# Kernel optimization log

Measured on AMD Instinct MI355X. Metric: run time of the kernel, lower is better.

Reference implementation:

```python
import jax, jax.numpy as jnp
import numpy as np

N = 50000   # total nodes across batched graphs
E = 800000  # total edges
F = 30      # input node features
G = 256     # number of graphs in the disjoint batch
CH = [128, 64, 32]
N_LABELS = 2


def setup_inputs() -> dict:
    key = jax.random.key(0)
    ks = jax.random.split(key, 16)
    x = jax.random.normal(ks[0], (N, F), dtype=jnp.float32)
    edge_weight = jax.random.uniform(ks[1], (E,), dtype=jnp.float32)
    edge_row = jax.random.randint(ks[2], (E,), 0, N, dtype=jnp.int32)
    edge_col = jax.random.randint(ks[3], (E,), 0, N, dtype=jnp.int32)
    seg = jnp.sort(jax.random.randint(ks[4], (N,), 0, G, dtype=jnp.int32))
    # GCSConv params: out = A @ (x W1) + x W2 + b, per layer
    dims = [F] + CH
    params = {}
    kk = 5
    for l in range(3):
        fin, fout = dims[l], dims[l + 1]
        s = 1.0 / np.sqrt(fin)
        params[f"w1_{l+1}"] = jax.random.uniform(ks[kk], (fin, fout), minval=-s, maxval=s, dtype=jnp.float32); kk += 1
        params[f"w2_{l+1}"] = jax.random.uniform(ks[kk], (fin, fout), minval=-s, maxval=s, dtype=jnp.float32); kk += 1
        params[f"b_{l+1}"] = jnp.zeros((fout,), dtype=jnp.float32)
    sd = 1.0 / np.sqrt(CH[-1])
    params["wd"] = jax.random.uniform(ks[kk], (CH[-1], N_LABELS), minval=-sd, maxval=sd, dtype=jnp.float32)
    params["bd"] = jnp.zeros((N_LABELS,), dtype=jnp.float32)
    return {"x": x, "edge_weight": edge_weight, "edge_row": edge_row,
            "edge_col": edge_col, "seg": seg, **params}


def _gcs_conv(x, ew, er, ec, w1, w2, b):
    # spektral GCSConv: relu(A @ (x W1) + x W2 + b) with sparse A in COO form
    h = x @ w1                                   # [N, Fout]
    msgs = ew[:, None] * h[ec]                   # gather along edges [E, Fout]
    agg = jax.ops.segment_sum(msgs, er, num_segments=N)  # SpMM scatter [N, Fout]
    return jax.nn.relu(agg + x @ w2 + b)


def reference(x, edge_weight, edge_row, edge_col, seg,
              w1_1, w2_1, b_1, w1_2, w2_2, b_2, w1_3, w2_3, b_3, wd, bd):
    h = _gcs_conv(x, edge_weight, edge_row, edge_col, w1_1, w2_1, b_1)
    h = _gcs_conv(h, edge_weight, edge_row, edge_col, w1_2, w2_2, b_2)
    h = _gcs_conv(h, edge_weight, edge_row, edge_col, w1_3, w2_3, b_3)
    # GlobalAvgPool: segment mean over graph ids
    sums = jax.ops.segment_sum(h, seg, num_segments=G)               # [G, 32]
    cnts = jax.ops.segment_sum(jnp.ones((N,), h.dtype), seg, num_segments=G)
    pooled = sums / jnp.maximum(cnts, 1.0)[:, None]
    return jax.nn.softmax(pooled @ wd + bd, axis=-1)                 # [G, 2]
```

## Files before the change

kernel.cpp:

```cpp
#include <hip/hip_runtime.h>
#include <hip/hip_fp16.h>

#define N_NODES 50000
#define N_EDGES 800000
#define N_GRAPHS 256
#define NCB 196
#define CHUNK 3125
#define MBLK 782

typedef _Float16 f16x8 __attribute__((ext_vector_type(8)));
typedef float    f32x4 __attribute__((ext_vector_type(4)));

__global__ __launch_bounds__(256)
void hist_prep(const int* __restrict__ ER, const float* __restrict__ X,
               const int* __restrict__ SEG,
               const float* __restrict__ W1, const float* __restrict__ W2,
               const float* __restrict__ W12, const float* __restrict__ W22,
               const float* __restrict__ W13, const float* __restrict__ W23,
               int* __restrict__ ghist, __half* __restrict__ XPh,
               int* __restrict__ start,
               __half* __restrict__ W1f, __half* __restrict__ W2f,
               __half* __restrict__ W3f)
{
    int b = blockIdx.x;
    int t = threadIdx.x;
    if (b < 256) {
        __shared__ int h[NCB];
        for (int i = t; i < NCB; i += 256) h[i] = 0;
        __syncthreads();
        int lo = b * CHUNK, hi = lo + CHUNK;
        for (int e = lo + t; e < hi; e += 256) atomicAdd(&h[ER[e] >> 8], 1);
        __syncthreads();
        for (int i = t; i < NCB; i += 256) ghist[i * 256 + b] = h[i];
        return;
    }
    int bid = b - 256;
    if (bid < 6250) {
        int idx = bid * 256 + t;
        int n = idx >> 5;
        int c = idx & 31;
        float v = (c < 30) ? X[n * 30 + c] : 0.f;
        XPh[(size_t)n * 32 + c] = __float2half(v);
    } else if (bid < 6446) {
        int n = (bid - 6250) * 256 + t;
        if (n >= N_NODES) return;
        int g = SEG[n];
        int gprev = (n == 0) ? -1 : SEG[n - 1];
        for (int gg = gprev + 1; gg <= g; ++gg) start[gg] = n;
        if (n == N_NODES - 1)
            for (int gg = g + 1; gg <= N_GRAPHS; ++gg) start[gg] = N_NODES;
    } else {
        int idx = (bid - 6446) * 256 + t;
        if (idx < 8192) {
            int i = idx & 7, c = (idx >> 3) & 15, g = (idx >> 7) & 3;
            int s = (idx >> 9) & 1, n = idx >> 10;
            int k = s * 32 + g * 8 + i, col = n * 16 + c;
            float w = 0.f;
            if (k < 30) w = W1[k * 128 + col];
            else if (k >= 32 && k < 62) w = W2[(k - 32) * 128 + col];
            W1f[idx] = __float2half(w);
        } else if (idx < 24576) {
            int o = idx - 8192;
            int i = o & 7, c = (o >> 3) & 15, g = (o >> 7) & 3;
            int s = (o >> 9) & 3, n = o >> 11;
            int k = s * 32 + g * 8 + i, col = n * 16 + c;
            float w = (col < 64) ? W12[k * 64 + col] : W22[k * 64 + col - 64];
            W2f[o] = __float2half(w);
        } else {
            int o = idx - 24576;
            int i = o & 7, c = (o >> 3) & 15, g = (o >> 7) & 3;
            int s = (o >> 9) & 1, n = o >> 10;
            int k = s * 32 + g * 8 + i, col = n * 16 + c;
            float w = (col < 32) ? W13[k * 32 + col] : W23[k * 32 + col - 32];
            W3f[o] = __float2half(w);
        }
    }
}

__global__ __launch_bounds__(256)
void scan1(int* __restrict__ ghist, int* __restrict__ bsum)
{
    __shared__ int s[256];
    int t = threadIdx.x, b = blockIdx.x;
    int i = b * 256 + t;
    int v = ghist[i];
    s[t] = v;
    __syncthreads();
    for (int off = 1; off < 256; off <<= 1) {
        int u = (t >= off) ? s[t - off] : 0;
        __syncthreads();
        s[t] += u;
        __syncthreads();
    }
    ghist[i] = s[t] - v;
    if (t == 255) bsum[b] = s[255];
}

__global__ __launch_bounds__(256)
void c_scatter(const int* __restrict__ ER, const int* __restrict__ EC,
               const float* __restrict__ EW, const int* __restrict__ ghist,
               const int* __restrict__ bsum, unsigned int* __restrict__ tmp_sd,
               __half* __restrict__ tmp_w)
{
    __shared__ int s[256];
    __shared__ int cur[NCB];
    int t = threadIdx.x, blk = blockIdx.x;
    int v = (t < NCB) ? bsum[t] : 0;
    s[t] = v;
    __syncthreads();
    for (int off = 1; off < 256; off <<= 1) {
        int u = (t >= off) ? s[t - off] : 0;
        __syncthreads();
        s[t] += u;
        __syncthreads();
    }
    if (t < NCB) cur[t] = (s[t] - v) + ghist[t * 256 + blk];
    __syncthreads();
    int lo = blk * CHUNK, hi = lo + CHUNK;
    for (int e = lo + t; e < hi; e += 256) {
        int d = ER[e];
        int pos = atomicAdd(&cur[d >> 8], 1);
        tmp_sd[pos] = (unsigned int)EC[e] | ((unsigned int)(d & 255) << 16);
        tmp_w[pos] = __float2half(EW[e]);
    }
}

__device__ __forceinline__ void fma8h(float4& a0, float4& a1, float w,
                                      const uint4& raw)
{
    const __half2* hp = (const __half2*)&raw;
    float2 f0 = __half22float2(hp[0]);
    float2 f1 = __half22float2(hp[1]);
    float2 f2 = __half22float2(hp[2]);
    float2 f3 = __half22float2(hp[3]);
    a0.x = fmaf(w, f0.x, a0.x); a0.y = fmaf(w, f0.y, a0.y);
    a0.z = fmaf(w, f1.x, a0.z); a0.w = fmaf(w, f1.y, a0.w);
    a1.x = fmaf(w, f2.x, a1.x); a1.y = fmaf(w, f2.y, a1.y);
    a1.z = fmaf(w, f3.x, a1.z); a1.w = fmaf(w, f3.y, a1.w);
}

__device__ __forceinline__ unsigned int relu2(unsigned int u)
{
    unsigned int lo = (u & 0x8000u)     ? 0u : (u & 0x0000FFFFu);
    unsigned int hi = (u & 0x80000000u) ? 0u : (u & 0xFFFF0000u);
    return lo | hi;
}

__global__ __launch_bounds__(1024)
void bsort(const unsigned int* __restrict__ tmp_sd, const __half* __restrict__ tmp_w,
           const int* __restrict__ bsum,
           unsigned int* __restrict__ packed, int* __restrict__ rowptr)
{
    __shared__ int s[256];
    __shared__ int hist[256];
    __shared__ int cur[256];
    int t = threadIdx.x, b = blockIdx.x;

    if (t < 256) s[t] = (t < NCB) ? bsum[t] : 0;
    __syncthreads();
    for (int off = 1; off < 256; off <<= 1) {
        int u = 0;
        if (t < 256 && t >= off) u = s[t - off];
        __syncthreads();
        if (t < 256) s[t] += u;
        __syncthreads();
    }
    int cntb = bsum[b];
    int base = s[b] - cntb;
    int end  = base + cntb;
    __syncthreads();

    if (t < 256) hist[t] = 0;
    __syncthreads();
    for (int j = base + t; j < end; j += 1024)
        atomicAdd(&hist[(tmp_sd[j] >> 16) & 255], 1);
    __syncthreads();
    int hv = 0;
    if (t < 256) { hv = hist[t]; s[t] = hv; }
    __syncthreads();
    for (int off = 1; off < 256; off <<= 1) {
        int u = 0;
        if (t < 256 && t >= off) u = s[t - off];
        __syncthreads();
        if (t < 256) s[t] += u;
        __syncthreads();
    }
    if (t < 256) {
        int excl = s[t] - hv;
        int n = b * 256 + t;
        if (n < N_NODES) rowptr[n] = base + excl;
        if (b == NCB - 1 && t == 0) rowptr[N_NODES] = N_EDGES;
        cur[t] = base + excl;
    }
    __syncthreads();
    for (int j = base + t; j < end; j += 1024) {
        unsigned int sd = tmp_sd[j];
        unsigned short hb = __half_as_ushort(tmp_w[j]);
        int pos = atomicAdd(&cur[(sd >> 16) & 255], 1);
        packed[pos] = (sd & 0xFFFF) | ((unsigned int)hb << 16);
    }
}

__global__ __launch_bounds__(256)
void dense12_mfma(const __half* __restrict__ XPh, const int* __restrict__ rowptr,
                  const unsigned int* __restrict__ packed,
                  const __half* __restrict__ W1f, const float* __restrict__ B1,
                  const __half* __restrict__ W2f, const float* __restrict__ B2,
                  __half* __restrict__ H2h, __half* __restrict__ A2h)
{
    __shared__ __align__(16) __half As[64 * 72];
    __shared__ __align__(16) __half Hs[64 * 136];
    const int tid = threadIdx.x;
    const int m0 = blockIdx.x * 64;
    const int lane = tid & 63;
    const int w  = tid >> 6;
    const int lr = lane & 15;
    const int lg = lane >> 4;

    {
        int row = tid >> 2, c4 = tid & 3;
        int gm = m0 + row;
        uint4 v = make_uint4(0, 0, 0, 0);
        if (gm < N_NODES) v = *(const uint4*)(XPh + (size_t)gm * 32 + c4 * 8);
        *(uint4*)(As + row * 72 + (4 + c4) * 8) = v;
    }
    {
        int local = tid >> 2, q = tid & 3;
        int n = m0 + local;
        __half2 hb2[4];
        if (n < N_NODES) {
            int r0 = rowptr[n], r1 = rowptr[n + 1];
            float4 acc0 = make_float4(0.f, 0.f, 0.f, 0.f);
            float4 acc1 = make_float4(0.f, 0.f, 0.f, 0.f);
            int j = r0;
            for (; j + 3 < r1; j += 4) {
                unsigned int ra = packed[j],     rb = packed[j + 1];
                unsigned int rc = packed[j + 2], rd = packed[j + 3];
                uint4 rawa = *(const uint4*)(XPh + (size_t)(ra & 0xFFFF) * 32 + q * 8);
                uint4 rawb = *(const uint4*)(XPh + (size_t)(rb & 0xFFFF) * 32 + q * 8);
                uint4 rawc = *(const uint4*)(XPh + (size_t)(rc & 0xFFFF) * 32 + q * 8);
                uint4 rawd = *(const uint4*)(XPh + (size_t)(rd & 0xFFFF) * 32 + q * 8);
                float wa = __half2float(__ushort_as_half((unsigned short)(ra >> 16)));
                float wb = __half2float(__ushort_as_half((unsigned short)(rb >> 16)));
                float wc = __half2float(__ushort_as_half((unsigned short)(rc >> 16)));
                float wd = __half2float(__ushort_as_half((unsigned short)(rd >> 16)));
                fma8h(acc0, acc1, wa, rawa);
                fma8h(acc0, acc1, wb, rawb);
                fma8h(acc0, acc1, wc, rawc);
                fma8h(acc0, acc1, wd, rawd);
            }
            for (; j < r1; ++j) {
                unsigned int r = packed[j];
                uint4 raw = *(const uint4*)(XPh + (size_t)(r & 0xFFFF) * 32 + q * 8);
                float wv = __half2float(__ushort_as_half((unsigned short)(r >> 16)));
                fma8h(acc0, acc1, wv, raw);
            }
            hb2[0] = __float22half2_rn(make_float2(acc0.x, acc0.y));
            hb2[1] = __float22half2_rn(make_float2(acc0.z, acc0.w));
            hb2[2] = __float22half2_rn(make_float2(acc1.x, acc1.y));
            hb2[3] = __float22half2_rn(make_float2(acc1.z, acc1.w));
        } else {
            hb2[0] = hb2[1] = hb2[2] = hb2[3] = __float22half2_rn(make_float2(0.f, 0.f));
        }
        *(uint4*)(As + local * 72 + q * 8) = *(uint4*)&hb2[0];
    }
    __syncthreads();

    f32x4 acc[4][2];
    #pragma unroll
    for (int m = 0; m < 4; ++m)
        #pragma unroll
        for (int j = 0; j < 2; ++j)
            acc[m][j] = (f32x4){0.f, 0.f, 0.f, 0.f};

    #pragma unroll
    for (int s = 0; s < 2; ++s) {
        f16x8 a[4];
        #pragma unroll
        for (int m = 0; m < 4; ++m)
            a[m] = *(const f16x8*)(As + (m * 16 + lr) * 72 + s * 32 + lg * 8);
        #pragma unroll
        for (int j = 0; j < 2; ++j) {
            const int n = 2 * w + j;
            f16x8 b = *(const f16x8*)(W1f + (((n * 2 + s) * 4 + lg) * 16 + lr) * 8);
            #pragma unroll
            for (int m = 0; m < 4; ++m)
                acc[m][j] = __builtin_amdgcn_mfma_f32_16x16x32_f16(a[m], b, acc[m][j], 0, 0, 0);
        }
    }

    #pragma unroll
    for (int j = 0; j < 2; ++j) {
        const int n = 2 * w + j;
        const float bias = B1[n * 16 + lr];
        #pragma unroll
        for (int m = 0; m < 4; ++m)
            #pragma unroll
            for (int r = 0; r < 4; ++r) {
                float v = fmaxf(acc[m][j][r] + bias, 0.f);
                Hs[(m * 16 + lg * 4 + r) * 136 + n * 16 + lr] = __float2half(v);
            }
    }
    __syncthreads();

    f32x4 acc2[4][2];
    #pragma unroll
    for (int m = 0; m < 4; ++m)
        #pragma unroll
        for (int j = 0; j < 2; ++j)
            acc2[m][j] = (f32x4){0.f, 0.f, 0.f, 0.f};

    #pragma unroll
    for (int s = 0; s < 4; ++s) {
        f16x8 a[4];
        #pragma unroll
        for (int m = 0; m < 4; ++m)
            a[m] = *(const f16x8*)(Hs + (m * 16 + lr) * 136 + s * 32 + lg * 8);
        #pragma unroll
        for (int j = 0; j < 2; ++j) {
            const int n = 2 * w + j;
            f16x8 b = *(const f16x8*)(W2f + (((n * 4 + s) * 4 + lg) * 16 + lr) * 8);
            #pragma unroll
            for (int m = 0; m < 4; ++m)
                acc2[m][j] = __builtin_amdgcn_mfma_f32_16x16x32_f16(a[m], b, acc2[m][j], 0, 0, 0);
        }
    }
    __syncthreads();

    #pragma unroll
    for (int j = 0; j < 2; ++j) {
        const int n = 2 * w + j;
        const float bias = (n >= 4) ? B2[(n - 4) * 16 + lr] : 0.f;
        #pragma unroll
        for (int m = 0; m < 4; ++m)
            #pragma unroll
            for (int r = 0; r < 4; ++r)
                Hs[(m * 16 + lg * 4 + r) * 136 + n * 16 + lr] =
                    __float2half(acc2[m][j][r] + bias);
    }
    __syncthreads();

    for (int idx = tid; idx < 1024; idx += 256) {
        int row = idx >> 4, c8 = idx & 15;
        int gm = m0 + row;
        if (gm < N_NODES) {
            uint4 v = *(const uint4*)(Hs + row * 136 + c8 * 8);
            if (c8 < 8) *(uint4*)(H2h + (size_t)gm * 64 + c8 * 8) = v;
            else        *(uint4*)(A2h + (size_t)gm * 64 + (c8 - 8) * 8) = v;
        }
    }
}

__global__ __launch_bounds__(256)
void dense3_mfma(const __half* __restrict__ X, const __half* __restrict__ W3f,
                 const float* __restrict__ B3, __half* __restrict__ H3h,
                 __half* __restrict__ B2h)
{
    __shared__ __align__(16) __half As[64 * 72];
    __shared__ __align__(16) __half Os[64 * 72];
    const int tid = threadIdx.x;
    const int m0 = blockIdx.x * 64;
    const int lane = tid & 63;
    const int w  = tid >> 6;
    const int lr = lane & 15;
    const int lg = lane >> 4;

    for (int idx = tid; idx < 512; idx += 256) {
        int row = idx >> 3, c8 = idx & 7;
        int gm = m0 + row;
        uint4 v = make_uint4(0, 0, 0, 0);
        if (gm < N_NODES) v = *(const uint4*)(X + (size_t)gm * 64 + c8 * 8);
        v.x = relu2(v.x); v.y = relu2(v.y); v.z = relu2(v.z); v.w = relu2(v.w);
        *(uint4*)(As + row * 72 + c8 * 8) = v;
    }
    __syncthreads();

    f32x4 acc[4];
    #pragma unroll
    for (int m = 0; m < 4; ++m) acc[m] = (f32x4){0.f, 0.f, 0.f, 0.f};

    #pragma unroll
    for (int s = 0; s < 2; ++s) {
        f16x8 b = *(const f16x8*)(W3f + (((w * 2 + s) * 4 + lg) * 16 + lr) * 8);
        #pragma unroll
        for (int m = 0; m < 4; ++m) {
            f16x8 a = *(const f16x8*)(As + (m * 16 + lr) * 72 + s * 32 + lg * 8);
            acc[m] = __builtin_amdgcn_mfma_f32_16x16x32_f16(a, b, acc[m], 0, 0, 0);
        }
    }

    const float bias = (w >= 2) ? B3[(w - 2) * 16 + lr] : 0.f;
    #pragma unroll
    for (int m = 0; m < 4; ++m)
        #pragma unroll
        for (int r = 0; r < 4; ++r)
            Os[(m * 16 + lg * 4 + r) * 72 + w * 16 + lr] =
                __float2half(acc[m][r] + bias);
    __syncthreads();

    for (int idx = tid; idx < 512; idx += 256) {
        int row = idx >> 3, c8 = idx & 7;
        int gm = m0 + row;
        if (gm < N_NODES) {
            uint4 v = *(const uint4*)(Os + row * 72 + c8 * 8);
            if (c8 < 4) *(uint4*)(H3h + (size_t)gm * 32 + c8 * 8) = v;
            else        *(uint4*)(B2h + (size_t)gm * 32 + (c8 - 4) * 8) = v;
        }
    }
}

template<int FOUT, int S>
__global__ __launch_bounds__(512)
void spmm_split(const __half* __restrict__ H, const int* __restrict__ rowptr,
                const unsigned int* __restrict__ packed, __half* __restrict__ AGGh)
{
    constexpr int T = FOUT / 8;
    constexpr int NPB = 512 / (S * T);
    __shared__ float part[NPB][S - 1][FOUT + 4];
    int tid = threadIdx.x;
    int local = tid / (S * T);
    int rem = tid % (S * T);
    int s = rem / T;
    int q = rem % T;
    int n = blockIdx.x * NPB + local;
    bool valid = (n < N_NODES);
    float4 acc0 = make_float4(0.f, 0.f, 0.f, 0.f);
    float4 acc1 = make_float4(0.f, 0.f, 0.f, 0.f);
    __half* ap = AGGh + (size_t)n * FOUT + q * 8;
    if (valid) {
        int r0 = rowptr[n], r1 = rowptr[n + 1];
        int deg = r1 - r0;
        int lo = r0 + (deg * s) / S;
        int hi = r0 + (deg * (s + 1)) / S;
        if (s == 0) {
            uint4 raw = *(const uint4*)ap;
            const __half2* hp = (const __half2*)&raw;
            float2 f0 = __half22float2(hp[0]);
            float2 f1 = __half22float2(hp[1]);
            float2 f2 = __half22float2(hp[2]);
            float2 f3 = __half22float2(hp[3]);
            acc0 = make_float4(f0.x, f0.y, f1.x, f1.y);
            acc1 = make_float4(f2.x, f2.y, f3.x, f3.y);
        }
        int j = lo;
        for (; j + 3 < hi; j += 4) {
            unsigned int ra = packed[j],     rb = packed[j + 1];
            unsigned int rc = packed[j + 2], rd = packed[j + 3];
            uint4 rawa = *(const uint4*)(H + (size_t)(ra & 0xFFFF) * FOUT + q * 8);
            uint4 rawb = *(const uint4*)(H + (size_t)(rb & 0xFFFF) * FOUT + q * 8);
            uint4 rawc = *(const uint4*)(H + (size_t)(rc & 0xFFFF) * FOUT + q * 8);
            uint4 rawd = *(const uint4*)(H + (size_t)(rd & 0xFFFF) * FOUT + q * 8);
            float wa = __half2float(__ushort_as_half((unsigned short)(ra >> 16)));
            float wb = __half2float(__ushort_as_half((unsigned short)(rb >> 16)));
            float wc = __half2float(__ushort_as_half((unsigned short)(rc >> 16)));
            float wd = __half2float(__ushort_as_half((unsigned short)(rd >> 16)));
            fma8h(acc0, acc1, wa, rawa);
            fma8h(acc0, acc1, wb, rawb);
            fma8h(acc0, acc1, wc, rawc);
            fma8h(acc0, acc1, wd, rawd);
        }
        for (; j < hi; ++j) {
            unsigned int r = packed[j];
            uint4 raw = *(const uint4*)(H + (size_t)(r & 0xFFFF) * FOUT + q * 8);
            float w = __half2float(__ushort_as_half((unsigned short)(r >> 16)));
            fma8h(acc0, acc1, w, raw);
        }
    }
    if (s > 0) {
        *(float4*)&part[local][s - 1][q * 8 + 0] = acc0;
        *(float4*)&part[local][s - 1][q * 8 + 4] = acc1;
    }
    __syncthreads();
    if (s == 0 && valid) {
        #pragma unroll
        for (int ss = 0; ss < S - 1; ++ss) {
            float4 p0 = *(float4*)&part[local][ss][q * 8 + 0];
            float4 p1 = *(float4*)&part[local][ss][q * 8 + 4];
            acc0.x += p0.x; acc0.y += p0.y; acc0.z += p0.z; acc0.w += p0.w;
            acc1.x += p1.x; acc1.y += p1.y; acc1.z += p1.z; acc1.w += p1.w;
        }
        __half2 hb[4];
        hb[0] = __float22half2_rn(make_float2(acc0.x, acc0.y));
        hb[1] = __float22half2_rn(make_float2(acc0.z, acc0.w));
        hb[2] = __float22half2_rn(make_float2(acc1.x, acc1.y));
        hb[3] = __float22half2_rn(make_float2(acc1.z, acc1.w));
        *(uint4*)ap = *(uint4*)&hb[0];
    }
}

__global__ __launch_bounds__(1024)
void pool_kernel(const __half* __restrict__ H, const int* __restrict__ start,
                 const float* __restrict__ WD, const float* __restrict__ BD,
                 float* __restrict__ OUT)
{
    __shared__ float red[32][33];
    int g = blockIdx.x;
    int s = start[g], e = start[g + 1];
    int q = threadIdx.x & 31;
    int grp = threadIdx.x >> 5;
    float acc = 0.f;
    for (int n = s + grp; n < e; n += 32)
        acc += fmaxf(__half2float(H[(size_t)n * 32 + q]), 0.f);
    red[grp][q] = acc;
    __syncthreads();
    if (threadIdx.x < 32) {
        float v = 0.f;
        #pragma unroll
        for (int i = 0; i < 32; ++i) v += red[i][q];
        float inv = (e > s) ? 1.0f / (float)(e - s) : 1.0f;
        float p = v * inv;
        float p0 = p * WD[q * 2 + 0];
        float p1 = p * WD[q * 2 + 1];
        #pragma unroll
        for (int off = 16; off; off >>= 1) {
            p0 += __shfl_down(p0, off, 32);
            p1 += __shfl_down(p1, off, 32);
        }
        if (q == 0) {
            float l0 = p0 + BD[0], l1 = p1 + BD[1];
            float m = fmaxf(l0, l1);
            float e0 = expf(l0 - m), e1 = expf(l1 - m);
            float si = 1.0f / (e0 + e1);
            OUT[g * 2 + 0] = e0 * si;
            OUT[g * 2 + 1] = e1 * si;
        }
    }
}

extern "C" void kernel_launch(void* const* d_in, const int* in_sizes, int n_in,
                              void* d_out, int out_size, void* d_ws, size_t ws_size,
                              hipStream_t stream)
{
    const float* x    = (const float*)d_in[0];
    const float* ew   = (const float*)d_in[1];
    const int*   er   = (const int*)d_in[2];
    const int*   ec   = (const int*)d_in[3];
    const int*   seg  = (const int*)d_in[4];
    const float* w1_1 = (const float*)d_in[5];
    const float* w2_1 = (const float*)d_in[6];
    const float* b_1  = (const float*)d_in[7];
    const float* w1_2 = (const float*)d_in[8];
    const float* w2_2 = (const float*)d_in[9];
    const float* b_2  = (const float*)d_in[10];
    const float* w1_3 = (const float*)d_in[11];
    const float* w2_3 = (const float*)d_in[12];
    const float* b_3  = (const float*)d_in[13];
    const float* wd   = (const float*)d_in[14];
    const float* bd   = (const float*)d_in[15];

    float* ws = (float*)d_ws;
    int*   IW = (int*)d_ws;
    __half* XPh    = (__half*)ws;
    unsigned int* tmp_sd = (unsigned int*)(ws + 1600000);
    __half* tmp_w  = (__half*)(ws + 2400000);
    __half* H2h    = (__half*)(ws + 3200000);
    __half* A2h    = (__half*)(ws + 4800000);
    __half* H3h    = (__half*)(ws + 6400000);
    __half* B2h    = (__half*)(ws + 7200000);
    unsigned int* packed = (unsigned int*)(IW + 8000000);
    int*    rowptr = IW + 9000000;
    int*    ghist  = IW + 9060000;
    int*    bsum   = IW + 9115000;
    int*    start  = IW + 9120000;
    __half* W1f    = (__half*)(ws + 9125000);
    __half* W2f    = (__half*)(ws + 9130000);
    __half* W3f    = (__half*)(ws + 9139000);

    dim3 blk(256);

    hist_prep<<<dim3(256 + 6558), blk, 0, stream>>>(er, x, seg, w1_1, w2_1,
                                                    w1_2, w2_2, w1_3, w2_3,
                                                    ghist, XPh, start,
                                                    W1f, W2f, W3f);
    scan1<<<dim3(NCB), blk, 0, stream>>>(ghist, bsum);
    c_scatter<<<dim3(256), blk, 0, stream>>>(er, ec, ew, ghist, bsum, tmp_sd, tmp_w);
    bsort<<<dim3(NCB), dim3(1024), 0, stream>>>(tmp_sd, tmp_w, bsum, packed, rowptr);

    dense12_mfma<<<dim3(MBLK), blk, 0, stream>>>(XPh, rowptr, packed, W1f, b_1,
                                                 W2f, b_2, H2h, A2h);
    spmm_split<64, 4><<<dim3((N_NODES + 15) / 16), dim3(512), 0, stream>>>(H2h, rowptr,
                                                                           packed, A2h);
    dense3_mfma<<<dim3(MBLK), blk, 0, stream>>>(A2h, W3f, b_3, H3h, B2h);
    spmm_split<32, 4><<<dim3((N_NODES + 31) / 32), dim3(512), 0, stream>>>(H3h, rowptr,
                                                                           packed, B2h);

    pool_kernel<<<dim3(N_GRAPHS), dim3(1024), 0, stream>>>(B2h, start, wd, bd,
                                                           (float*)d_out);
}
```

Before: 174.7 us.

## Split edge aggregation across two thread halves in dense12 and vectorize feature prep

The first fused kernel now runs at 512 threads. Each node's edge list is split between two thread groups, with partial sums combined through shared memory, and each wave computes one MFMA column tile instead of two. The X-to-half conversion writes eight packed halves per thread with one vector store, which shrinks its grid. The source/weight temporaries of the edge sort are merged into one uint2 array, so each edge costs one store and one load. Together these aim to raise parallelism in the latency-bound gather and cut memory transactions. The cost is an extra barrier and shared-memory reduction, plus lower per-thread work in the MFMA stage.

```diff
diff --git a/kernel.cpp b/kernel.cpp
--- a/kernel.cpp
+++ b/kernel.cpp
@@ -35,14 +35,22 @@
         return;
     }
     int bid = b - 256;
-    if (bid < 6250) {
+    if (bid < 782) {
         int idx = bid * 256 + t;
-        int n = idx >> 5;
-        int c = idx & 31;
-        float v = (c < 30) ? X[n * 30 + c] : 0.f;
-        XPh[(size_t)n * 32 + c] = __float2half(v);
-    } else if (bid < 6446) {
-        int n = (bid - 6250) * 256 + t;
+        int n = idx >> 2;
+        int c4 = idx & 3;
+        if (n >= N_NODES) return;
+        __half2 hb[4];
+        #pragma unroll
+        for (int k = 0; k < 4; ++k) {
+            int c0 = c4 * 8 + 2 * k;
+            float v0 = (c0 < 30) ? X[n * 30 + c0] : 0.f;
+            float v1 = (c0 + 1 < 30) ? X[n * 30 + c0 + 1] : 0.f;
+            hb[k] = __float22half2_rn(make_float2(v0, v1));
+        }
+        *(uint4*)(XPh + (size_t)n * 32 + c4 * 8) = *(uint4*)&hb[0];
+    } else if (bid < 978) {
+        int n = (bid - 782) * 256 + t;
         if (n >= N_NODES) return;
         int g = SEG[n];
         int gprev = (n == 0) ? -1 : SEG[n - 1];
@@ -50,7 +58,7 @@
         if (n == N_NODES - 1)
             for (int gg = g + 1; gg <= N_GRAPHS; ++gg) start[gg] = N_NODES;
     } else {
-        int idx = (bid - 6446) * 256 + t;
+        int idx = (bid - 978) * 256 + t;
         if (idx < 8192) {
             int i = idx & 7, c = (idx >> 3) & 15, g = (idx >> 7) & 3;
             int s = (idx >> 9) & 1, n = idx >> 10;
@@ -99,8 +107,7 @@
 __global__ __launch_bounds__(256)
 void c_scatter(const int* __restrict__ ER, const int* __restrict__ EC,
                const float* __restrict__ EW, const int* __restrict__ ghist,
-               const int* __restrict__ bsum, unsigned int* __restrict__ tmp_sd,
-               __half* __restrict__ tmp_w)
+               const int* __restrict__ bsum, uint2* __restrict__ tmp)
 {
     __shared__ int s[256];
     __shared__ int cur[NCB];
@@ -120,8 +127,8 @@
     for (int e = lo + t; e < hi; e += 256) {
         int d = ER[e];
         int pos = atomicAdd(&cur[d >> 8], 1);
-        tmp_sd[pos] = (unsigned int)EC[e] | ((unsigned int)(d & 255) << 16);
-        tmp_w[pos] = __float2half(EW[e]);
+        tmp[pos] = make_uint2((unsigned int)EC[e] | ((unsigned int)(d & 255) << 16),
+                              (unsigned int)__half_as_ushort(__float2half(EW[e])));
     }
 }
 
@@ -147,8 +154,7 @@
 }
 
 __global__ __launch_bounds__(1024)
-void bsort(const unsigned int* __restrict__ tmp_sd, const __half* __restrict__ tmp_w,
-           const int* __restrict__ bsum,
+void bsort(const uint2* __restrict__ tmp, const int* __restrict__ bsum,
            unsigned int* __restrict__ packed, int* __restrict__ rowptr)
 {
     __shared__ int s[256];
@@ -173,7 +179,7 @@
     if (t < 256) hist[t] = 0;
     __syncthreads();
     for (int j = base + t; j < end; j += 1024)
-        atomicAdd(&hist[(tmp_sd[j] >> 16) & 255], 1);
+        atomicAdd(&hist[(tmp[j].x >> 16) & 255], 1);
     __syncthreads();
     int hv = 0;
     if (t < 256) { hv = hist[t]; s[t] = hv; }
@@ -194,14 +200,13 @@
     }
     __syncthreads();
     for (int j = base + t; j < end; j += 1024) {
-        unsigned int sd = tmp_sd[j];
-        unsigned short hb = __half_as_ushort(tmp_w[j]);
-        int pos = atomicAdd(&cur[(sd >> 16) & 255], 1);
-        packed[pos] = (sd & 0xFFFF) | ((unsigned int)hb << 16);
-    }
-}
-
-__global__ __launch_bounds__(256)
+        uint2 v = tmp[j];
+        int pos = atomicAdd(&cur[(v.x >> 16) & 255], 1);
+        packed[pos] = (v.x & 0xFFFF) | (v.y << 16);
+    }
+}
+
+__global__ __launch_bounds__(512)
 void dense12_mfma(const __half* __restrict__ XPh, const int* __restrict__ rowptr,
                   const unsigned int* __restrict__ packed,
                   const __half* __restrict__ W1f, const float* __restrict__ B1,
@@ -212,12 +217,8 @@
     __shared__ __align__(16) __half Hs[64 * 136];
     const int tid = threadIdx.x;
     const int m0 = blockIdx.x * 64;
-    const int lane = tid & 63;
-    const int w  = tid >> 6;
-    const int lr = lane & 15;
-    const int lg = lane >> 4;
-
-    {
+
+    if (tid < 256) {
         int row = tid >> 2, c4 = tid & 3;
         int gm = m0 + row;
         uint4 v = make_uint4(0, 0, 0, 0);
@@ -225,15 +226,19 @@
         *(uint4*)(As + row * 72 + (4 + c4) * 8) = v;
     }
     {
-        int local = tid >> 2, q = tid & 3;
+        int local = tid >> 3;
+        int es = (tid >> 2) & 1;
+        int q = tid & 3;
         int n = m0 + local;
-        __half2 hb2[4];
+        float4 acc0 = make_float4(0.f, 0.f, 0.f, 0.f);
+        float4 acc1 = make_float4(0.f, 0.f, 0.f, 0.f);
         if (n < N_NODES) {
             int r0 = rowptr[n], r1 = rowptr[n + 1];
-            float4 acc0 = make_float4(0.f, 0.f, 0.f, 0.f);
-            float4 acc1 = make_float4(0.f, 0.f, 0.f, 0.f);
-            int j = r0;
-            for (; j + 3 < r1; j += 4) {
+            int mid = (r0 + r1) >> 1;
+            int lo = es ? mid : r0;
+            int hi = es ? r1 : mid;
+            int j = lo;
+            for (; j + 3 < hi; j += 4) {
                 unsigned int ra = packed[j],     rb = packed[j + 1];
                 unsigned int rc = packed[j + 2], rd = packed[j + 3];
                 uint4 rawa = *(const uint4*)(XPh + (size_t)(ra & 0xFFFF) * 32 + q * 8);
@@ -249,98 +254,92 @@
                 fma8h(acc0, acc1, wc, rawc);
                 fma8h(acc0, acc1, wd, rawd);
             }
-            for (; j < r1; ++j) {
+            for (; j < hi; ++j) {
                 unsigned int r = packed[j];
                 uint4 raw = *(const uint4*)(XPh + (size_t)(r & 0xFFFF) * 32 + q * 8);
                 float wv = __half2float(__ushort_as_half((unsigned short)(r >> 16)));
                 fma8h(acc0, acc1, wv, raw);
             }
+        }
+        float* part = (float*)Hs;
+        if (es == 1) {
+            *(float4*)&part[local * 36 + q * 8 + 0] = acc0;
+            *(float4*)&part[local * 36 + q * 8 + 4] = acc1;
+        }
+        __syncthreads();
+        if (es == 0) {
+            float4 p0 = *(float4*)&part[local * 36 + q * 8 + 0];
+            float4 p1 = *(float4*)&part[local * 36 + q * 8 + 4];
+            acc0.x += p0.x; acc0.y += p0.y; acc0.z += p0.z; acc0.w += p0.w;
+            acc1.x += p1.x; acc1.y += p1.y; acc1.z += p1.z; acc1.w += p1.w;
+            __half2 hb2[4];
             hb2[0] = __float22half2_rn(make_float2(acc0.x, acc0.y));
             hb2[1] = __float22half2_rn(make_float2(acc0.z, acc0.w));
             hb2[2] = __float22half2_rn(make_float2(acc1.x, acc1.y));
             hb2[3] = __float22half2_rn(make_float2(acc1.z, acc1.w));
-        } else {
-            hb2[0] = hb2[1] = hb2[2] = hb2[3] = __float22half2_rn(make_float2(0.f, 0.f));
-        }
-        *(uint4*)(As + local * 72 + q * 8) = *(uint4*)&hb2[0];
-    }
-    __syncthreads();
-
-    f32x4 acc[4][2];
-    #pragma unroll
-    for (int m = 0; m < 4; ++m)
-        #pragma unroll
-        for (int j = 0; j < 2; ++j)
-            acc[m][j] = (f32x4){0.f, 0.f, 0.f, 0.f};
+            *(uint4*)(As + local * 72 + q * 8) = *(uint4*)&hb2[0];
+        }
+    }
+    __syncthreads();
+
+    const int lane = tid & 63;
+    const int w  = tid >> 6;
+    const int lr = lane & 15;
+    const int lg = lane >> 4;
+
+    f32x4 acc[4];
+    #pragma unroll
+    for (int m = 0; m < 4; ++m) acc[m] = (f32x4){0.f, 0.f, 0.f, 0.f};
 
     #pragma unroll
     for (int s = 0; s < 2; ++s) {
-        f16x8 a[4];
-        #pragma unroll
-        for (int m = 0; m < 4; ++m)
-            a[m] = *(const f16x8*)(As + (m * 16 + lr) * 72 + s * 32 + lg * 8);
-        #pragma unroll
-        for (int j = 0; j < 2; ++j) {
-            const int n = 2 * w + j;
-            f16x8 b = *(const f16x8*)(W1f + (((n * 2 + s) * 4 + lg) * 16 + lr) * 8);
-            #pragma unroll
-            for (int m = 0; m < 4; ++m)
-                acc[m][j] = __builtin_amdgcn_mfma_f32_16x16x32_f16(a[m], b, acc[m][j], 0, 0, 0);
-        }
-    }
-
-    #pragma unroll
-    for (int j = 0; j < 2; ++j) {
-        const int n = 2 * w + j;
-        const float bias = B1[n * 16 + lr];
+        f16x8 b = *(const f16x8*)(W1f + (((w * 2 + s) * 4 + lg) * 16 + lr) * 8);
+        #pragma unroll
+        for (int m = 0; m < 4; ++m) {
+            f16x8 a = *(const f16x8*)(As + (m * 16 + lr) * 72 + s * 32 + lg * 8);
+            acc[m] = __builtin_amdgcn_mfma_f32_16x16x32_f16(a, b, acc[m], 0, 0, 0);
+        }
+    }
+
+    {
+        const float bias = B1[w * 16 + lr];
         #pragma unroll
         for (int m = 0; m < 4; ++m)
             #pragma unroll
             for (int r = 0; r < 4; ++r) {
-                float v = fmaxf(acc[m][j][r] + bias, 0.f);
-                Hs[(m * 16 + lg * 4 + r) * 136 + n * 16 + lr] = __float2half(v);
+                float v = fmaxf(acc[m][r] + bias, 0.f);
+                Hs[(m * 16 + lg * 4 + r) * 136 + w * 16 + lr] = __float2half(v);
             }
     }
     __syncthreads();
 
-    f32x4 acc2[4][2];
-    #pragma unroll
-    for (int m = 0; m < 4; ++m)
-        #pragma unroll
-        for (int j = 0; j < 2; ++j)
-            acc2[m][j] = (f32x4){0.f, 0.f, 0.f, 0.f};
+    f32x4 acc2[4];
+    #pragma unroll
+    for (int m = 0; m < 4; ++m) acc2[m] = (f32x4){0.f, 0.f, 0.f, 0.f};
 
     #pragma unroll
     for (int s = 0; s < 4; ++s) {
-        f16x8 a[4];
-        #pragma unroll
-        for (int m = 0; m < 4; ++m)
-            a[m] = *(const f16x8*)(Hs + (m * 16 + lr) * 136 + s * 32 + lg * 8);
-        #pragma unroll
-        for (int j = 0; j < 2; ++j) {
-            const int n = 2 * w + j;
-            f16x8 b = *(const f16x8*)(W2f + (((n * 4 + s) * 4 + lg) * 16 + lr) * 8);
-            #pragma unroll
-            for (int m = 0; m < 4; ++m)
-                acc2[m][j] = __builtin_amdgcn_mfma_f32_16x16x32_f16(a[m], b, acc2[m][j], 0, 0, 0);
-        }
-    }
-    __syncthreads();
-
-    #pragma unroll
-    for (int j = 0; j < 2; ++j) {
-        const int n = 2 * w + j;
-        const float bias = (n >= 4) ? B2[(n - 4) * 16 + lr] : 0.f;
+        f16x8 b = *(const f16x8*)(W2f + (((w * 4 + s) * 4 + lg) * 16 + lr) * 8);
+        #pragma unroll
+        for (int m = 0; m < 4; ++m) {
+            f16x8 a = *(const f16x8*)(Hs + (m * 16 + lr) * 136 + s * 32 + lg * 8);
+            acc2[m] = __builtin_amdgcn_mfma_f32_16x16x32_f16(a, b, acc2[m], 0, 0, 0);
+        }
+    }
+    __syncthreads();
+
+    {
+        const float bias = (w >= 4) ? B2[(w - 4) * 16 + lr] : 0.f;
         #pragma unroll
         for (int m = 0; m < 4; ++m)
             #pragma unroll
             for (int r = 0; r < 4; ++r)
-                Hs[(m * 16 + lg * 4 + r) * 136 + n * 16 + lr] =
-                    __float2half(acc2[m][j][r] + bias);
-    }
-    __syncthreads();
-
-    for (int idx = tid; idx < 1024; idx += 256) {
+                Hs[(m * 16 + lg * 4 + r) * 136 + w * 16 + lr] =
+                    __float2half(acc2[m][r] + bias);
+    }
+    __syncthreads();
+
+    for (int idx = tid; idx < 1024; idx += 512) {
         int row = idx >> 4, c8 = idx & 15;
         int gm = m0 + row;
         if (gm < N_NODES) {
@@ -551,8 +550,7 @@
     float* ws = (float*)d_ws;
     int*   IW = (int*)d_ws;
     __half* XPh    = (__half*)ws;
-    unsigned int* tmp_sd = (unsigned int*)(ws + 1600000);
-    __half* tmp_w  = (__half*)(ws + 2400000);
+    uint2*  tmp    = (uint2*)(ws + 1600000);
     __half* H2h    = (__half*)(ws + 3200000);
     __half* A2h    = (__half*)(ws + 4800000);
     __half* H3h    = (__half*)(ws + 6400000);
@@ -568,16 +566,16 @@
 
     dim3 blk(256);
 
-    hist_prep<<<dim3(256 + 6558), blk, 0, stream>>>(er, x, seg, w1_1, w2_1,
-                                                    w1_2, w2_2, w1_3, w2_3,
-                                                    ghist, XPh, start,
-                                                    W1f, W2f, W3f);
+    hist_prep<<<dim3(256 + 782 + 196 + 112), blk, 0, stream>>>(
+        er, x, seg, w1_1, w2_1, w1_2, w2_2, w1_3, w2_3,
+        ghist, XPh, start, W1f, W2f, W3f);
     scan1<<<dim3(NCB), blk, 0, stream>>>(ghist, bsum);
-    c_scatter<<<dim3(256), blk, 0, stream>>>(er, ec, ew, ghist, bsum, tmp_sd, tmp_w);
-    bsort<<<dim3(NCB), dim3(1024), 0, stream>>>(tmp_sd, tmp_w, bsum, packed, rowptr);
-
-    dense12_mfma<<<dim3(MBLK), blk, 0, stream>>>(XPh, rowptr, packed, W1f, b_1,
-                                                 W2f, b_2, H2h, A2h);
+    c_scatter<<<dim3(256), blk, 0, stream>>>(er, ec, ew, ghist, bsum, tmp);
+    bsort<<<dim3(NCB), dim3(1024), 0, stream>>>(tmp, bsum, packed, rowptr);
+
+    dense12_mfma<<<dim3(MBLK), dim3(512), 0, stream>>>(XPh, rowptr, packed,
+                                                       W1f, b_1, W2f, b_2,
+                                                       H2h, A2h);
     spmm_split<64, 4><<<dim3((N_NODES + 15) / 16), dim3(512), 0, stream>>>(H2h, rowptr,
                                                                            packed, A2h);
     dense3_mfma<<<dim3(MBLK), blk, 0, stream>>>(A2h, W3f, b_3, H3h, B2h);
```

Measured after the change: 172.8 us. No clear change (-1.1%).
